# Performance work log

Hardware: AMD Instinct MI355X
Metric: run time of the kernel (lower is better)

## Reference

```python
import jax, jax.numpy as jnp
import numpy as np

M, K, N = 8192, 4096, 4096
DIV = 1.0 / (127.0 * 127.0)


def setup_inputs() -> dict:
    key = jax.random.key(0)
    k1, k2, k3, k4, k5 = jax.random.split(key, 5)
    x = jax.random.randint(k1, (M, K), -127, 128, dtype=jnp.int8)
    weight_int8 = jax.random.randint(k2, (N, K), -127, 128, dtype=jnp.int8)
    scale_x = jnp.abs(jax.random.normal(k3, (M,), dtype=jnp.float32)) * 0.01
    scale_w = jnp.abs(jax.random.normal(k4, (N,), dtype=jnp.float32)) * 0.01
    bias = (jax.random.normal(k5, (N,), dtype=jnp.float32) * 0.01).astype(jnp.float16)
    return {"x": x, "scale_x": scale_x, "weight_int8": weight_int8,
            "scale_w": scale_w, "bias": bias}


def reference(x, scale_x, weight_int8, scale_w, bias):
    # int8 GEMM with int32 accumulation: [M,K] @ [K,N]
    acc = jax.lax.dot_general(
        x, weight_int8.T,
        dimension_numbers=(((1,), (0,)), ((), ())),
        preferred_element_type=jnp.int32,
    ).astype(jnp.float32)
    # fused rowwise/colwise dequant + bias, cast to fp16
    out = acc * DIV * scale_x[:, None] * scale_w[None, :] + bias.astype(jnp.float32)[None, :]
    return out.astype(jnp.float16)
```

## Files before the change

kernel.cpp:

```cpp
#include <hip/hip_runtime.h>
#include <hip/hip_fp16.h>
#include <cstdint>
#include <cstddef>

#define M_DIM 8192
#define N_DIM 4096
#define K_DIM 4096

typedef int v4i __attribute__((ext_vector_type(4)));

__global__ __launch_bounds__(256) void pack_i32_to_i8(const int* __restrict__ src,
                                                      uint8_t* __restrict__ dst,
                                                      int n16) {
    int i = blockIdx.x * 256 + threadIdx.x;
    if (i >= n16) return;
    const int4* s = (const int4*)src + (size_t)i * 4;
    int4 a = s[0], b = s[1], c = s[2], d = s[3];
    uint32_t p0 = (a.x & 0xff) | ((a.y & 0xff) << 8) | ((a.z & 0xff) << 16) | ((uint32_t)(a.w & 0xff) << 24);
    uint32_t p1 = (b.x & 0xff) | ((b.y & 0xff) << 8) | ((b.z & 0xff) << 16) | ((uint32_t)(b.w & 0xff) << 24);
    uint32_t p2 = (c.x & 0xff) | ((c.y & 0xff) << 8) | ((c.z & 0xff) << 16) | ((uint32_t)(c.w & 0xff) << 24);
    uint32_t p3 = (d.x & 0xff) | ((d.y & 0xff) << 8) | ((d.z & 0xff) << 16) | ((uint32_t)(d.w & 0xff) << 24);
    ((uint4*)dst)[i] = make_uint4(p0, p1, p2, p3);
}

__device__ __forceinline__ void gload_lds16(const void* g, void* l) {
    __builtin_amdgcn_global_load_lds(
        (const __attribute__((address_space(1))) void*)g,
        (__attribute__((address_space(3))) void*)l,
        16, 0, 0);
}

__global__ __launch_bounds__(256) void gemm_i8_dq(const int8_t* __restrict__ A,
                                                  const int8_t* __restrict__ W,
                                                  const float* __restrict__ sx,
                                                  const float* __restrict__ sw,
                                                  const float* __restrict__ bias,
                                                  float* __restrict__ out) {
    __shared__ int8_t sA[128 * 64];
    __shared__ int8_t sB[128 * 64];

    const int t    = threadIdx.x;
    const int lane = t & 63;
    const int wave = t >> 6;
    const int wm   = wave >> 1;
    const int wn   = wave & 1;
    const int bm   = blockIdx.y;
    const int bn   = blockIdx.x;

    const int srow = t >> 2;
    const int scol = (t & 3) * 16;
    const int8_t* gA0 = A + (size_t)(bm * 128 + srow) * K_DIM + scol;
    const int8_t* gA1 = A + (size_t)(bm * 128 + 64 + srow) * K_DIM + scol;
    const int8_t* gB0 = W + (size_t)(bn * 128 + srow) * K_DIM + scol;
    const int8_t* gB1 = W + (size_t)(bn * 128 + 64 + srow) * K_DIM + scol;
    int8_t* lA0 = &sA[t * 16];
    int8_t* lA1 = &sA[4096 + t * 16];
    int8_t* lB0 = &sB[t * 16];
    int8_t* lB1 = &sB[4096 + t * 16];

    const int frow_a = wm * 64 + (lane & 15);
    const int frow_b = wn * 64 + (lane & 15);
    const int koff   = (lane >> 4) * 16;

    v4i acc[4][4];
    const v4i vzero = {0, 0, 0, 0};
#pragma unroll
    for (int mi = 0; mi < 4; mi++)
#pragma unroll
        for (int ni = 0; ni < 4; ni++) acc[mi][ni] = vzero;

    for (int kt = 0; kt < K_DIM; kt += 64) {
        __syncthreads();
        gload_lds16(gA0 + kt, lA0);
        gload_lds16(gA1 + kt, lA1);
        gload_lds16(gB0 + kt, lB0);
        gload_lds16(gB1 + kt, lB1);
        __syncthreads();

        v4i af[4], bf[4];
#pragma unroll
        for (int i = 0; i < 4; i++) {
            af[i] = *(const v4i*)(&sA[(frow_a + i * 16) * 64 + koff]);
            bf[i] = *(const v4i*)(&sB[(frow_b + i * 16) * 64 + koff]);
        }
#pragma unroll
        for (int mi = 0; mi < 4; mi++)
#pragma unroll
            for (int ni = 0; ni < 4; ni++)
                acc[mi][ni] = __builtin_amdgcn_mfma_i32_16x16x64_i8(
                    af[mi], bf[ni], acc[mi][ni], 0, 0, 0);
    }

    const float DIVF = (float)(1.0 / (127.0 * 127.0));
    const int col0 = bn * 128 + wn * 64 + (lane & 15);
    const int row0 = bm * 128 + wm * 64 + (lane >> 4) * 4;

    float swv[4], bv[4];
#pragma unroll
    for (int ni = 0; ni < 4; ni++) {
        swv[ni] = sw[col0 + ni * 16];
        bv[ni]  = bias[col0 + ni * 16];
    }

#pragma unroll
    for (int mi = 0; mi < 4; mi++) {
#pragma unroll
        for (int r = 0; r < 4; r++) {
            const int row = row0 + mi * 16 + r;
            const float xs = sx[row];
#pragma unroll
            for (int ni = 0; ni < 4; ni++) {
                float v = __fmul_rn((float)acc[mi][ni][r], DIVF);
                v = __fmul_rn(v, xs);
                v = __fmul_rn(v, swv[ni]);
                v = __fadd_rn(v, bv[ni]);
                out[(size_t)row * N_DIM + col0 + ni * 16] = __half2float(__float2half(v));
            }
        }
    }
}

extern "C" void kernel_launch(void* const* d_in, const int* in_sizes, int n_in,
                              void* d_out, int out_size, void* d_ws, size_t ws_size,
                              hipStream_t stream) {
    const int*   x_i32 = (const int*)d_in[0];
    const float* sx    = (const float*)d_in[1];
    const int*   w_i32 = (const int*)d_in[2];
    const float* sw    = (const float*)d_in[3];
    const float* bias  = (const float*)d_in[4];
    float* out = (float*)d_out;

    uint8_t* xb = (uint8_t*)d_ws;
    uint8_t* wb = (uint8_t*)d_ws + (size_t)M_DIM * K_DIM;

    const int nx16 = (M_DIM * K_DIM) / 16;
    const int nw16 = (N_DIM * K_DIM) / 16;
    pack_i32_to_i8<<<(nx16 + 255) / 256, 256, 0, stream>>>(x_i32, xb, nx16);
    pack_i32_to_i8<<<(nw16 + 255) / 256, 256, 0, stream>>>(w_i32, wb, nw16);

    dim3 grid(N_DIM / 128, M_DIM / 128);
    gemm_i8_dq<<<grid, 256, 0, stream>>>((const int8_t*)xb, (const int8_t*)wb,
                                         sx, sw, bias, out);
}
```

Before: 428.2 us.

## Use MFMA-fragment LDS layout with K=128 tiles and simpler pack kernel

The GEMM now stages K tiles of 128 instead of 64 per barrier pair, halving the number of sync/load phases. Global-to-LDS loads write each 16x64 sub-block in the exact per-lane fragment order, so the fragment reads become contiguous lane*16 loads without bank conflicts. The pack kernel now packs one int4 per thread instead of four, giving more threads with smaller per-thread work. LDS use doubles to 32 KB per block, which may reduce occupancy.

```diff
diff --git a/kernel.cpp b/kernel.cpp
--- a/kernel.cpp
+++ b/kernel.cpp
@@ -10,24 +10,19 @@
 typedef int v4i __attribute__((ext_vector_type(4)));
 
 __global__ __launch_bounds__(256) void pack_i32_to_i8(const int* __restrict__ src,
-                                                      uint8_t* __restrict__ dst,
-                                                      int n16) {
+                                                      uint32_t* __restrict__ dst,
+                                                      int n4) {
     int i = blockIdx.x * 256 + threadIdx.x;
-    if (i >= n16) return;
-    const int4* s = (const int4*)src + (size_t)i * 4;
-    int4 a = s[0], b = s[1], c = s[2], d = s[3];
-    uint32_t p0 = (a.x & 0xff) | ((a.y & 0xff) << 8) | ((a.z & 0xff) << 16) | ((uint32_t)(a.w & 0xff) << 24);
-    uint32_t p1 = (b.x & 0xff) | ((b.y & 0xff) << 8) | ((b.z & 0xff) << 16) | ((uint32_t)(b.w & 0xff) << 24);
-    uint32_t p2 = (c.x & 0xff) | ((c.y & 0xff) << 8) | ((c.z & 0xff) << 16) | ((uint32_t)(c.w & 0xff) << 24);
-    uint32_t p3 = (d.x & 0xff) | ((d.y & 0xff) << 8) | ((d.z & 0xff) << 16) | ((uint32_t)(d.w & 0xff) << 24);
-    ((uint4*)dst)[i] = make_uint4(p0, p1, p2, p3);
+    if (i >= n4) return;
+    int4 a = ((const int4*)src)[i];
+    dst[i] = (uint32_t)(a.x & 0xff) | ((uint32_t)(a.y & 0xff) << 8) |
+             ((uint32_t)(a.z & 0xff) << 16) | ((uint32_t)a.w << 24);
 }
 
-__device__ __forceinline__ void gload_lds16(const void* g, void* l) {
+__device__ __forceinline__ void gload_lds16(const int8_t* g, int8_t* l) {
     __builtin_amdgcn_global_load_lds(
         (const __attribute__((address_space(1))) void*)g,
-        (__attribute__((address_space(3))) void*)l,
-        16, 0, 0);
+        (__attribute__((address_space(3))) void*)l, 16, 0, 0);
 }
 
 __global__ __launch_bounds__(256) void gemm_i8_dq(const int8_t* __restrict__ A,
@@ -36,31 +31,31 @@
                                                   const float* __restrict__ sw,
                                                   const float* __restrict__ bias,
                                                   float* __restrict__ out) {
-    __shared__ int8_t sA[128 * 64];
-    __shared__ int8_t sB[128 * 64];
+    __shared__ int8_t sA[128 * 128];
+    __shared__ int8_t sB[128 * 128];
 
     const int t    = threadIdx.x;
     const int lane = t & 63;
-    const int wave = t >> 6;
-    const int wm   = wave >> 1;
-    const int wn   = wave & 1;
+    const int w    = t >> 6;
+    const int wm   = w >> 1;
+    const int wn   = w & 1;
     const int bm   = blockIdx.y;
     const int bn   = blockIdx.x;
+    const int r16  = lane & 15;
+    const int c16  = lane >> 4;
 
-    const int srow = t >> 2;
-    const int scol = (t & 3) * 16;
-    const int8_t* gA0 = A + (size_t)(bm * 128 + srow) * K_DIM + scol;
-    const int8_t* gA1 = A + (size_t)(bm * 128 + 64 + srow) * K_DIM + scol;
-    const int8_t* gB0 = W + (size_t)(bn * 128 + srow) * K_DIM + scol;
-    const int8_t* gB1 = W + (size_t)(bn * 128 + 64 + srow) * K_DIM + scol;
-    int8_t* lA0 = &sA[t * 16];
-    int8_t* lA1 = &sA[4096 + t * 16];
-    int8_t* lB0 = &sB[t * 16];
-    int8_t* lB1 = &sB[4096 + t * 16];
-
-    const int frow_a = wm * 64 + (lane & 15);
-    const int frow_b = wn * 64 + (lane & 15);
-    const int koff   = (lane >> 4) * 16;
+    const int8_t* gA[4]; const int8_t* gB[4];
+    int8_t* lA[4]; int8_t* lB[4];
+#pragma unroll
+    for (int j = 0; j < 4; j++) {
+        const int sgrp = j & 1;
+        const int ksub = j >> 1;
+        const int s    = sgrp * 4 + w;
+        gA[j] = A + (size_t)(bm * 128 + s * 16 + r16) * K_DIM + ksub * 64 + c16 * 16;
+        gB[j] = W + (size_t)(bn * 128 + s * 16 + r16) * K_DIM + ksub * 64 + c16 * 16;
+        lA[j] = &sA[(ksub * 8 + s) * 1024 + lane * 16];
+        lB[j] = &sB[(ksub * 8 + s) * 1024 + lane * 16];
+    }
 
     v4i acc[4][4];
     const v4i vzero = {0, 0, 0, 0};
@@ -69,26 +64,30 @@
 #pragma unroll
         for (int ni = 0; ni < 4; ni++) acc[mi][ni] = vzero;
 
-    for (int kt = 0; kt < K_DIM; kt += 64) {
+    for (int kt = 0; kt < K_DIM; kt += 128) {
         __syncthreads();
-        gload_lds16(gA0 + kt, lA0);
-        gload_lds16(gA1 + kt, lA1);
-        gload_lds16(gB0 + kt, lB0);
-        gload_lds16(gB1 + kt, lB1);
+#pragma unroll
+        for (int j = 0; j < 4; j++) {
+            gload_lds16(gA[j] + kt, lA[j]);
+            gload_lds16(gB[j] + kt, lB[j]);
+        }
         __syncthreads();
 
-        v4i af[4], bf[4];
 #pragma unroll
-        for (int i = 0; i < 4; i++) {
-            af[i] = *(const v4i*)(&sA[(frow_a + i * 16) * 64 + koff]);
-            bf[i] = *(const v4i*)(&sB[(frow_b + i * 16) * 64 + koff]);
+        for (int kk = 0; kk < 2; kk++) {
+            v4i af[4], bf[4];
+#pragma unroll
+            for (int i = 0; i < 4; i++) {
+                af[i] = *(const v4i*)(&sA[(kk * 8 + wm * 4 + i) * 1024 + lane * 16]);
+                bf[i] = *(const v4i*)(&sB[(kk * 8 + wn * 4 + i) * 1024 + lane * 16]);
+            }
+#pragma unroll
+            for (int mi = 0; mi < 4; mi++)
+#pragma unroll
+                for (int ni = 0; ni < 4; ni++)
+                    acc[mi][ni] = __builtin_amdgcn_mfma_i32_16x16x64_i8(
+                        af[mi], bf[ni], acc[mi][ni], 0, 0, 0);
         }
-#pragma unroll
-        for (int mi = 0; mi < 4; mi++)
-#pragma unroll
-            for (int ni = 0; ni < 4; ni++)
-                acc[mi][ni] = __builtin_amdgcn_mfma_i32_16x16x64_i8(
-                    af[mi], bf[ni], acc[mi][ni], 0, 0, 0);
     }
 
     const float DIVF = (float)(1.0 / (127.0 * 127.0));
@@ -133,10 +132,10 @@
     uint8_t* xb = (uint8_t*)d_ws;
     uint8_t* wb = (uint8_t*)d_ws + (size_t)M_DIM * K_DIM;
 
-    const int nx16 = (M_DIM * K_DIM) / 16;
-    const int nw16 = (N_DIM * K_DIM) / 16;
-    pack_i32_to_i8<<<(nx16 + 255) / 256, 256, 0, stream>>>(x_i32, xb, nx16);
-    pack_i32_to_i8<<<(nw16 + 255) / 256, 256, 0, stream>>>(w_i32, wb, nw16);
+    const int nx4 = (M_DIM * K_DIM) / 4;
+    const int nw4 = (N_DIM * K_DIM) / 4;
+    pack_i32_to_i8<<<(nx4 + 255) / 256, 256, 0, stream>>>(x_i32, (uint32_t*)xb, nx4);
+    pack_i32_to_i8<<<(nw4 + 255) / 256, 256, 0, stream>>>(w_i32, (uint32_t*)wb, nw4);
 
     dim3 grid(N_DIM / 128, M_DIM / 128);
     gemm_i8_dq<<<grid, 256, 0, stream>>>((const int8_t*)xb, (const int8_t*)wb,
```

Result: slower. 502.4 us (+17.3%).
